# Kernel tuning notes

Measured on AMD Instinct MI355X. Metric: run time of the kernel, lower is better.

## Reference

```python
import jax, jax.numpy as jnp
import numpy as np
from jax import lax

SUB, NSUB, FRAME, COND, FEAT, PEMB = 40, 4, 160, 256, 20, 64
B, NB_FRAMES = 64, 100
T = NB_FRAMES + 4  # two valid k=3 convs drop 4 frames


def setup_inputs() -> dict:
    keys = iter(jax.random.split(jax.random.key(0), 40))
    def W(shape, fan_in):
        return jax.random.normal(next(keys), shape, jnp.float32) / np.float32(np.sqrt(fan_in))
    z = lambda *s: jnp.zeros(s, jnp.float32)
    inp = {
        'features': jax.random.normal(next(keys), (B, T, FEAT), jnp.float32),
        'period': jax.random.randint(next(keys), (B, T), 32, 256, jnp.int32),
        'nb_frames': NB_FRAMES,
        'rand_shift': jax.random.uniform(next(keys), (B, 1), jnp.float32),
        'pembed': 0.1 * jax.random.normal(next(keys), (256, PEMB), jnp.float32),
        'fd1_w': W((FEAT + PEMB, COND), FEAT + PEMB), 'fd1_b': z(COND),
        'conv1_w': W((COND, COND, 3), 3 * COND), 'conv1_b': z(COND),
        'conv2_w': W((COND, COND, 3), 3 * COND), 'conv2_b': z(COND),
        'fd2_w': W((COND, COND), COND), 'fd2_b': z(COND),
        'sd1_w': W((3 * SUB + COND, COND), 3 * SUB + COND), 'sd1_b': z(COND),
        'sd2_w': W((COND, COND), COND), 'sd2_b': z(COND),
        'g1_wi': W((COND, 3 * COND), COND), 'g1_bi': z(3 * COND),
        'g1_wh': W((COND, 3 * COND), COND), 'g1_bh': z(3 * COND),
        'g2_wi': W((COND, 3 * COND), COND), 'g2_bi': z(3 * COND),
        'g2_wh': W((COND, 3 * COND), COND), 'g2_bh': z(3 * COND),
        'g3_wi': W((COND, 3 * COND), COND), 'g3_bi': z(3 * COND),
        'g3_wh': W((COND, 3 * COND), COND), 'g3_bh': z(3 * COND),
        'out_w': W((COND, SUB), COND), 'out_b': z(SUB),
    }
    return inp


def _gru(x, h, wi, bi, wh, bh):
    # torch GRUCell gate order: r, z, n
    gi = x @ wi + bi
    gh = h @ wh + bh
    i_r, i_z, i_n = jnp.split(gi, 3, axis=1)
    h_r, h_z, h_n = jnp.split(gh, 3, axis=1)
    r = jax.nn.sigmoid(i_r + h_r)
    zt = jax.nn.sigmoid(i_z + h_z)
    n = jnp.tanh(i_n + r * h_n)
    return (1.0 - zt) * n + zt * h


def _conv1d_valid(x, w, b):
    # x: (B, C, T), w: (O, I, 3)
    y = lax.conv_general_dilated(x, w, (1,), 'VALID', dimension_numbers=('NCH', 'OIH', 'NCH'))
    return y + b[None, :, None]


def _forward(features, rand_shift, pembed, fd1_w, fd1_b, conv1_w, conv1_b, conv2_w, conv2_b,
             fd2_w, fd2_b, sd1_w, sd1_b, sd2_w, sd2_b,
             g1_wi, g1_bi, g1_wh, g1_bh, g2_wi, g2_bi, g2_wh, g2_bh, g3_wi, g3_bi, g3_wh, g3_bh,
             out_w, out_b, period, nb_frames):
    b = features.shape[0]
    two_pi = np.float32(2.0 * np.pi)
    # --- phase embedding (gen_phase_embedding on period[:, 3:-1]) ---
    p = period[:, 3:-1].astype(jnp.float32)              # (B, nb_frames)
    w0 = two_pi / p
    w0_shift = jnp.concatenate([two_pi * rand_shift / FRAME, w0[:, :-1]], axis=1)
    cum_phase = FRAME * jnp.cumsum(w0_shift, axis=1)     # (B, nb_frames)
    fine = w0[:, :, None] * jnp.arange(FRAME, dtype=jnp.float32)
    embed = (cum_phase[:, :, None] + fine).reshape(b, nb_frames * NSUB, SUB)
    phase_real = jnp.cos(embed)
    phase_imag = jnp.sin(embed)
    # --- conditioning network ---
    pe = pembed[period]                                  # (B, T, PEMB)
    t = jnp.tanh(jnp.concatenate([features, pe], axis=-1) @ fd1_w + fd1_b)
    x = t.transpose(0, 2, 1)                             # (B, COND, T)
    x = jnp.tanh(_conv1d_valid(x, conv1_w, conv1_b))
    x = jnp.tanh(_conv1d_valid(x, conv2_w, conv2_b))
    cond = jnp.tanh(x.transpose(0, 2, 1) @ fd2_w + fd2_b)  # (B, T-4, COND)
    cond_steps = jnp.repeat(cond[:, :nb_frames], NSUB, axis=1)  # (B, steps, COND)
    xs = (cond_steps.transpose(1, 0, 2), phase_real.transpose(1, 0, 2), phase_imag.transpose(1, 0, 2))
    h0 = jnp.zeros((b, COND), features.dtype)
    prev0 = jnp.zeros((b, SUB), features.dtype)

    def step(carry, inp):
        prev, h1, h2, h3 = carry
        c, pr, pi = inp
        tt = jnp.tanh(jnp.concatenate([c, prev, pr, pi], axis=1) @ sd1_w + sd1_b)
        tt = jnp.tanh(tt @ sd2_w + sd2_b)
        h1 = _gru(tt, h1, g1_wi, g1_bi, g1_wh, g1_bh)
        h2 = _gru(h1, h2, g2_wi, g2_bi, g2_wh, g2_bh)
        h3 = _gru(h2, h3, g3_wi, g3_bi, g3_wh, g3_bh)
        out = jnp.tanh(h3 @ out_w + out_b)
        return (out, h1, h2, h3), out

    (_, h1, h2, h3), outs = lax.scan(step, (prev0, h0, h0, h0), xs)
    sig = outs.transpose(1, 0, 2).reshape(b, -1)         # (B, nb_frames*FRAME)
    return sig, (h1, h2, h3)


def reference(features, period, nb_frames, rand_shift, pembed, fd1_w, fd1_b, conv1_w, conv1_b,
              conv2_w, conv2_b, fd2_w, fd2_b, sd1_w, sd1_b, sd2_w, sd2_b,
              g1_wi, g1_bi, g1_wh, g1_bh, g2_wi, g2_bi, g2_wh, g2_bh, g3_wi, g3_bi, g3_wh, g3_bh,
              out_w, out_b):
    return _forward(features, rand_shift, pembed, fd1_w, fd1_b, conv1_w, conv1_b, conv2_w, conv2_b,
                    fd2_w, fd2_b, sd1_w, sd1_b, sd2_w, sd2_b,
                    g1_wi, g1_bi, g1_wh, g1_bh, g2_wi, g2_bi, g2_wh, g2_bh,
                    g3_wi, g3_bi, g3_wh, g3_bh, out_w, out_b, period, nb_frames)
```

## Files before the change

kernel.cpp:

```cpp
#include <hip/hip_runtime.h>
#include <hip/hip_bf16.h>
#include <math.h>

#define B_ 64
#define T_ 104
#define FEAT_ 20
#define PEMB_ 64
#define COND_ 256
#define SUB_ 40
#define NBF_ 100
#define STEPS_ 400

typedef short short8 __attribute__((ext_vector_type(8)));
typedef float floatx4 __attribute__((ext_vector_type(4)));

__device__ inline unsigned short f2bf(float x){
  unsigned int u = __float_as_uint(x);
  unsigned int r = (u + 0x7fffu + ((u >> 16) & 1u)) >> 16;
  return (unsigned short)r;
}
__device__ inline float fast_tanh(float x){
  float e = __expf(2.f*x);
  return 1.f - 2.f*__builtin_amdgcn_rcpf(e + 1.f);
}
__device__ inline float fast_sigm(float x){
  return __builtin_amdgcn_rcpf(1.f + __expf(-x));
}
__device__ inline floatx4 mfma16(short8 a, short8 b, floatx4 c){
  return __builtin_amdgcn_mfma_f32_16x16x32_bf16(a, b, c, 0, 0, 0);
}
__device__ inline unsigned long long ld_coh_u64(const unsigned long long* p){
  return __hip_atomic_load(p, __ATOMIC_RELAXED, __HIP_MEMORY_SCOPE_AGENT);
}
__device__ inline unsigned int ld_coh_u32(const unsigned int* p){
  return __hip_atomic_load(p, __ATOMIC_RELAXED, __HIP_MEMORY_SCOPE_AGENT);
}
__device__ inline void st_coh_u32(unsigned int* p, unsigned int v){
  __hip_atomic_store(p, v, __ATOMIC_RELAXED, __HIP_MEMORY_SCOPE_AGENT);
}
__device__ inline void st_coh_u16(unsigned short* p, unsigned short v){
  unsigned int vv = v;
  asm volatile("global_store_short %0, %1, off sc0 sc1" :: "v"(p), "v"(vv) : "memory");
}

#define FLAG_IDX(st, g, sl) ((((st)*4 + (g))*16 + (sl))*16)

__device__ inline void wave0_wait(const unsigned int* fb, unsigned int tgt,
                                  int wave, int lane){
  if (wave == 0){
    for (;;){
      unsigned int v = 0xFFFFFFFFu;
      if (lane < 16) v = ld_coh_u32(fb + lane*16);
      #pragma unroll
      for (int off = 1; off < 64; off <<= 1)
        v = min(v, (unsigned int)__shfl_xor((int)v, off, 64));
      if (v >= tgt) break;
      __builtin_amdgcn_s_sleep(1);
    }
  }
}

__global__ void k_phase(const int* __restrict__ period, const float* __restrict__ rshift,
                        float* __restrict__ pr, float* __restrict__ pi){
  int b = blockIdx.x;
  __shared__ float cumf[NBF_], w0f[NBF_];
  if (threadIdx.x == 0){
    double acc = 2.0*M_PI*(double)rshift[b];
    for (int f = 0; f < NBF_; ++f){
      double w0 = 2.0*M_PI/(double)period[b*T_ + 3 + f];
      cumf[f] = (float)fmod(acc, 2.0*M_PI);
      w0f[f] = (float)w0;
      acc += 160.0*w0;
    }
  }
  __syncthreads();
  for (int e = threadIdx.x; e < NBF_*160; e += blockDim.x){
    int f = e/160, j = e - f*160;
    float ph = cumf[f] + w0f[f]*(float)j;
    int s = f*4 + j/40, u = j%40;
    pr[((size_t)b*STEPS_ + s)*SUB_ + u] = cosf(ph);
    pi[((size_t)b*STEPS_ + s)*SUB_ + u] = sinf(ph);
  }
}

__global__ void k_prep(const float* __restrict__ c1w, const float* __restrict__ c2w,
                       float* __restrict__ w1t, float* __restrict__ w2t,
                       unsigned int* __restrict__ flags, unsigned int* __restrict__ bufs){
  size_t tid = (size_t)blockIdx.x*blockDim.x + threadIdx.x;
  size_t nt = (size_t)gridDim.x*blockDim.x;
  for (size_t e = tid; e < 4096; e += nt) st_coh_u32(flags + e, 0u);
  for (size_t e = tid; e < 65536; e += nt) st_coh_u32(bufs + e, 0u);
  for (size_t e = tid; e < 768u*256u; e += nt){
    int kk = (int)(e >> 8), o = (int)(e & 255);
    int i = kk & 255, kc = kk >> 8;
    w1t[e] = c1w[(size_t)o*768 + i*3 + kc];
    w2t[e] = c2w[(size_t)o*768 + i*3 + kc];
  }
}

template<int MODE>
__global__ __launch_bounds__(256) void k_gemm(
    const float* __restrict__ a0, const float* __restrict__ a1, const float* __restrict__ a2,
    const int* __restrict__ ip,
    const float* __restrict__ Bm, const float* __restrict__ bias, float* __restrict__ C)
{
  constexpr int KT = (MODE==0) ? 6 : (MODE==1||MODE==2) ? 48 : (MODE==3) ? 16 : 21;
  __shared__ float As[16][68];
  __shared__ float Bs[16][68];
  int tid = threadIdx.x;
  int m0 = blockIdx.x*64, n0 = blockIdx.y*64;
  int tx = tid & 15, ty = tid >> 4;
  float acc[4][4] = {};
  int am = m0 + (tid >> 2);
  int akq = (tid & 3)*4;
  int bk = tid >> 4;
  int bn4 = (tid & 15)*4;

  for (int kt = 0; kt < KT; ++kt){
    int kbase = kt*16;
    float av[4];
    {
      int k0 = kbase + akq;
      if constexpr (MODE==0){
        if (k0 < 20){
          const float* p = a0 + (size_t)am*FEAT_ + k0;
          #pragma unroll
          for (int u=0;u<4;++u) av[u] = p[u];
        } else if (k0 < 84){
          const float* p = a1 + (size_t)ip[am]*PEMB_ + (k0-20);
          #pragma unroll
          for (int u=0;u<4;++u) av[u] = p[u];
        } else { av[0]=av[1]=av[2]=av[3]=0.f; }
      } else if constexpr (MODE==1){
        int b = am/102, t2 = am - b*102;
        int i = k0 & 255, kc = k0 >> 8;
        const float* p = a0 + ((size_t)(b*T_ + t2 + kc))*COND_ + i;
        #pragma unroll
        for (int u=0;u<4;++u) av[u] = p[u];
      } else if constexpr (MODE==2){
        int b = am/100, t2 = am - b*100;
        int i = k0 & 255, kc = k0 >> 8;
        const float* p = a0 + ((size_t)(b*102 + t2 + kc))*COND_ + i;
        #pragma unroll
        for (int u=0;u<4;++u) av[u] = p[u];
      } else if constexpr (MODE==3){
        const float* p = a0 + (size_t)am*COND_ + k0;
        #pragma unroll
        for (int u=0;u<4;++u) av[u] = p[u];
      } else {
        int b = am/400, s = am - b*400;
        const float* p;
        if (k0 < 256)      p = a0 + ((size_t)(b*100 + (s>>2)))*COND_ + k0;
        else if (k0 < 296) p = a1 + ((size_t)(b*400 + s))*SUB_ + (k0-256);
        else               p = a2 + ((size_t)(b*400 + s))*SUB_ + (k0-296);
        #pragma unroll
        for (int u=0;u<4;++u) av[u] = p[u];
      }
    }
    float bv[4];
    {
      int kB = kbase + bk;
      if constexpr (MODE==0){
        if (kB < 84){
          const float* p = Bm + (size_t)kB*256 + n0 + bn4;
          #pragma unroll
          for (int u=0;u<4;++u) bv[u] = p[u];
        } else { bv[0]=bv[1]=bv[2]=bv[3]=0.f; }
      } else if constexpr (MODE==4){
        int krow = (kB < 256) ? kB : kB + 40;
        const float* p = Bm + (size_t)krow*256 + n0 + bn4;
        #pragma unroll
        for (int u=0;u<4;++u) bv[u] = p[u];
      } else {
        const float* p = Bm + (size_t)kB*256 + n0 + bn4;
        #pragma unroll
        for (int u=0;u<4;++u) bv[u] = p[u];
      }
    }
    #pragma unroll
    for (int u=0;u<4;++u) As[akq+u][tid>>2] = av[u];
    #pragma unroll
    for (int u=0;u<4;++u) Bs[bk][bn4+u] = bv[u];
    __syncthreads();
    #pragma unroll
    for (int k = 0; k < 16; ++k){
      float a4[4], b4[4];
      #pragma unroll
      for (int i=0;i<4;++i) a4[i] = As[k][ty*4+i];
      #pragma unroll
      for (int j=0;j<4;++j) b4[j] = Bs[k][tx*4+j];
      #pragma unroll
      for (int i=0;i<4;++i)
        #pragma unroll
        for (int j=0;j<4;++j)
          acc[i][j] += a4[i]*b4[j];
    }
    __syncthreads();
  }
  #pragma unroll
  for (int i=0;i<4;++i){
    int m = m0 + ty*4 + i;
    #pragma unroll
    for (int j=0;j<4;++j){
      int n = n0 + tx*4 + j;
      float v = acc[i][j] + bias[n];
      if constexpr (MODE == 4){
        int b = m/400, s = m - b*400;
        C[((size_t)s*64 + b)*256 + n] = v;
      } else {
        C[(size_t)m*256 + n] = fast_tanh(v);
      }
    }
  }
}

__global__ __launch_bounds__(256, 1) void k_scan(
  const float* __restrict__ sd1_w, const float* __restrict__ sd2_w, const float* __restrict__ sd2_b,
  const float* __restrict__ g1_wi, const float* __restrict__ g1_bi, const float* __restrict__ g1_wh, const float* __restrict__ g1_bh,
  const float* __restrict__ g2_wi, const float* __restrict__ g2_bi, const float* __restrict__ g2_wh, const float* __restrict__ g2_bh,
  const float* __restrict__ g3_wi, const float* __restrict__ g3_bi, const float* __restrict__ g3_wh, const float* __restrict__ g3_bh,
  const float* __restrict__ out_w, const float* __restrict__ out_b,
  const float* __restrict__ tt1p,
  unsigned short* __restrict__ tt2buf, unsigned short* __restrict__ h1buf,
  unsigned short* __restrict__ h2buf, unsigned short* __restrict__ h3buf,
  unsigned int* __restrict__ flags, float* __restrict__ out)
{
  __shared__ __align__(16) char smem[65536];
  int tid = threadIdx.x;
  int lane = tid & 63, wave = tid >> 6;
  int q = lane >> 4, nI = lane & 15;
  int bI = blockIdx.x;
  int g = bI >> 6, rr = bI & 63;
  int set = rr >> 4, sl = rr & 15;
  int b0 = g*16;

  if (set == 0){
    char* outwF = smem;
    char* sd1p0 = smem + 24576;
    char* sd1p1 = smem + 40960;
    char* sd2F  = smem + 45056;
    char* stage = smem + 53248;
    char* prevl = smem + 61440;
    int col1 = sl*16 + nI;
    const unsigned int* fb3 = flags + FLAG_IDX(3, g, 0);
    unsigned int* myflag = flags + FLAG_IDX(0, g, sl);

    for (int t = wave; t < 24; t += 4){
      int nt = t >> 3, kk = t & 7;
      int c = nt*16 + nI;
      unsigned short v[8];
      #pragma unroll
      for (int j = 0; j < 8; ++j){
        int k = kk*32 + q*8 + j;
        v[j] = (c < 40) ? f2bf(out_w[(size_t)k*40 + c]) : (unsigned short)0;
      }
      *(short8*)(outwF + (t*64 + lane)*16) = *(short8*)v;
    }
    for (int t = wave; t < 16; t += 4){
      unsigned short v[8];
      #pragma unroll
      for (int j = 0; j < 8; ++j){
        int k = q*8 + j;
        v[j] = f2bf(sd1_w[(size_t)(256+k)*256 + t*16 + nI]);
      }
      *(short8*)(sd1p0 + (t*64 + lane)*16) = *(short8*)v;
    }
    {
      int nt = tid >> 4, ln = tid & 15;
      unsigned short v[8];
      #pragma unroll
      for (int j = 0; j < 8; ++j)
        v[j] = f2bf(sd1_w[(size_t)(256+32+j)*256 + nt*16 + ln]);
      *(short8*)(sd1p1 + tid*16) = *(short8*)v;
    }
    for (int t = wave; t < 8; t += 4){
      unsigned short v[8];
      #pragma unroll
      for (int j = 0; j < 8; ++j){
        int k = t*32 + q*8 + j;
        v[j] = f2bf(sd2_w[(size_t)k*256 + col1]);
      }
      *(short8*)(sd2F + (t*64 + lane)*16) = *(short8*)v;
    }
    for (int e = tid; e < 16*72; e += 256) *(unsigned short*)(prevl + e*2) = 0;
    float bout = 0.f;
    if (wave < 3){ int c = wave*16 + nI; if (c < 40) bout = out_b[c]; }
    float bsd2 = sd2_b[col1];
    __syncthreads();

    for (int s = 0; s <= STEPS_; ++s){
      float t1r[16];
      if (s < STEPS_){
        const float* tb = tt1p + ((size_t)s*64 + b0)*256;
        #pragma unroll
        for (int ii = 0; ii < 4; ++ii){
          int c = (wave*4 + ii)*16 + nI;
          #pragma unroll
          for (int i = 0; i < 4; ++i)
            t1r[ii*4+i] = tb[(q*4+i)*256 + c];
        }
      }
      if (s > 0){
        wave0_wait(fb3, (unsigned)s, wave, lane);
        __syncthreads();
        const unsigned short* h3s = h3buf + ((size_t)((s+1)&1)*4 + g)*4096;
        for (int c = tid; c < 512; c += 256){
          int row = c >> 5, gc = c & 31;
          const unsigned long long* sp = (const unsigned long long*)(h3s + row*256 + gc*8);
          unsigned long long w0 = ld_coh_u64(sp), w1 = ld_coh_u64(sp+1);
          unsigned long long* dst = (unsigned long long*)(stage + (row*32 + (gc ^ (row & 7)))*16);
          dst[0]=w0; dst[1]=w1;
        }
        __syncthreads();
        if (wave < 3){
          floatx4 acc = {0.f,0.f,0.f,0.f};
          #pragma unroll
          for (int kk = 0; kk < 8; ++kk){
            short8 a = *(const short8*)(stage + (nI*32 + ((kk*4+q) ^ (nI & 7)))*16);
            short8 b = *(const short8*)(outwF + ((wave*8+kk)*64 + lane)*16);
            acc = mfma16(a, b, acc);
          }
          int c = wave*16 + nI;
          #pragma unroll
          for (int i = 0; i < 4; ++i){
            int row = q*4 + i;
            float pv = (c < 40) ? fast_tanh(acc[i] + bout) : 0.f;
            *(unsigned short*)(prevl + (row*72 + c)*2) = f2bf(pv);
            if (sl == 0 && c < 40)
              out[(size_t)(b0+row)*16000 + (size_t)(s-1)*40 + c] = pv;
          }
        }
      }
      if (s == STEPS_) break;
      __syncthreads();
      #pragma unroll
      for (int ii = 0; ii < 4; ++ii){
        int nt = wave*4 + ii;
        floatx4 acc = {0.f,0.f,0.f,0.f};
        short8 a0v = *(const short8*)(prevl + nI*144 + q*16);
        short8 b0v = *(const short8*)(sd1p0 + (nt*64 + lane)*16);
        acc = mfma16(a0v, b0v, acc);
        short8 a1v = *(const short8*)(prevl + nI*144 + 64 + q*16);
        short8 b1v = {0,0,0,0,0,0,0,0};
        if (q == 0) b1v = *(const short8*)(sd1p1 + (nt*16 + nI)*16);
        acc = mfma16(a1v, b1v, acc);
        int c = nt*16 + nI;
        #pragma unroll
        for (int i = 0; i < 4; ++i){
          int row = q*4 + i;
          float tv = fast_tanh(acc[i] + t1r[ii*4+i]);
          int gc = c >> 3;
          *(unsigned short*)(stage + (row*32 + (gc ^ (row & 7)))*16 + (c & 7)*2) = f2bf(tv);
        }
      }
      __syncthreads();
      if (wave == 0){
        floatx4 acc = {0.f,0.f,0.f,0.f};
        #pragma unroll
        for (int kk = 0; kk < 8; ++kk){
          short8 a = *(const short8*)(stage + (nI*32 + ((kk*4+q) ^ (nI & 7)))*16);
          short8 b = *(const short8*)(sd2F + (kk*64 + lane)*16);
          acc = mfma16(a, b, acc);
        }
        unsigned short* t2 = tt2buf + ((size_t)(s&1)*4 + g)*4096;
        #pragma unroll
        for (int i = 0; i < 4; ++i){
          int row = q*4 + i;
          st_coh_u16(&t2[row*256 + col1], f2bf(fast_tanh(acc[i] + bsd2)));
        }
      }
      __syncthreads();
      if (tid == 0) st_coh_u32(myflag, (unsigned)(s+1));
    }
  } else {
    int gi_ = set - 1;
    const float* wi = (gi_==0) ? g1_wi : (gi_==1) ? g2_wi : g3_wi;
    const float* wh = (gi_==0) ? g1_wh : (gi_==1) ? g2_wh : g3_wh;
    const float* bi = (gi_==0) ? g1_bi : (gi_==1) ? g2_bi : g3_bi;
    const float* bh = (gi_==0) ? g1_bh : (gi_==1) ? g2_bh : g3_bh;
    unsigned short* hOut = (gi_==0) ? h1buf : (gi_==1) ? h2buf : h3buf;
    const unsigned short* xBase = (gi_==0) ? tt2buf : (gi_==1) ? h1buf : h2buf;
    char* wlds  = smem;
    char* stage = smem + 49152;
    int hc0 = sl*16;
    const unsigned int* fbOwn  = flags + FLAG_IDX(set, g, 0);
    const unsigned int* fbPrev = flags + FLAG_IDX(set-1, g, 0);
    unsigned int* myflag = flags + FLAG_IDX(set, g, sl);

    for (int t = wave; t < 48; t += 4){
      unsigned short v[8];
      #pragma unroll
      for (int j = 0; j < 8; ++j){
        float w;
        if (t < 32){
          int k512 = (t & 15)*32 + q*8 + j;
          int col = ((t < 16) ? 0 : 256) + hc0 + nI;
          w = (k512 < 256) ? wi[(size_t)k512*768 + col] : wh[(size_t)(k512-256)*768 + col];
        } else if (t < 40){
          int k = (t-32)*32 + q*8 + j;
          w = wi[(size_t)k*768 + 512 + hc0 + nI];
        } else {
          int k = (t-40)*32 + q*8 + j;
          w = wh[(size_t)k*768 + 512 + hc0 + nI];
        }
        v[j] = f2bf(w);
      }
      *(short8*)(wlds + (t*64 + lane)*16) = *(short8*)v;
    }
    float br = 0.f, bz = 0.f, bin = 0.f, bhn = 0.f;
    if (wave == 0){
      int cg = hc0 + nI;
      br  = bi[cg] + bh[cg];
      bz  = bi[256+cg] + bh[256+cg];
      bin = bi[512+cg];
      bhn = bh[512+cg];
    }
    floatx4 hst = {0.f,0.f,0.f,0.f};
    __syncthreads();

    for (int s = 0; s < STEPS_; ++s){
      if (s > 0) wave0_wait(fbOwn, (unsigned)s, wave, lane);
      __syncthreads();
      const unsigned short* hs = hOut + ((size_t)((s+1)&1)*4 + g)*4096;
      for (int c = tid; c < 512; c += 256){
        int row = c >> 5, gc = c & 31;
        const unsigned long long* sp = (const unsigned long long*)(hs + row*256 + gc*8);
        unsigned long long w0 = ld_coh_u64(sp), w1 = ld_coh_u64(sp+1);
        unsigned long long* dst = (unsigned long long*)(stage + (row*64 + ((32+gc) ^ (row & 7)))*16);
        dst[0]=w0; dst[1]=w1;
      }
      __syncthreads();
      floatx4 acc = {0.f,0.f,0.f,0.f};
      if (wave < 2){
        int tb = wave*16;
        #pragma unroll
        for (int kt = 8; kt < 16; ++kt){
          short8 a = *(const short8*)(stage + (nI*64 + ((kt*4+q) ^ (nI & 7)))*16);
          short8 b = *(const short8*)(wlds + ((tb+kt)*64 + lane)*16);
          acc = mfma16(a, b, acc);
        }
      } else if (wave == 3){
        #pragma unroll
        for (int kt = 0; kt < 8; ++kt){
          short8 a = *(const short8*)(stage + (nI*64 + ((32 + kt*4+q) ^ (nI & 7)))*16);
          short8 b = *(const short8*)(wlds + ((40+kt)*64 + lane)*16);
          acc = mfma16(a, b, acc);
        }
      }
      wave0_wait(fbPrev, (unsigned)(s+1), wave, lane);
      __syncthreads();
      const unsigned short* xs = xBase + ((size_t)(s&1)*4 + g)*4096;
      for (int c = tid; c < 512; c += 256){
        int row = c >> 5, gc = c & 31;
        const unsigned long long* sp = (const unsigned long long*)(xs + row*256 + gc*8);
        unsigned long long w0 = ld_coh_u64(sp), w1 = ld_coh_u64(sp+1);
        unsigned long long* dst = (unsigned long long*)(stage + (row*64 + (gc ^ (row & 7)))*16);
        dst[0]=w0; dst[1]=w1;
      }
      __syncthreads();
      if (wave < 2){
        int tb = wave*16;
        #pragma unroll
        for (int kt = 0; kt < 8; ++kt){
          short8 a = *(const short8*)(stage + (nI*64 + ((kt*4+q) ^ (nI & 7)))*16);
          short8 b = *(const short8*)(wlds + ((tb+kt)*64 + lane)*16);
          acc = mfma16(a, b, acc);
        }
      } else if (wave == 2){
        #pragma unroll
        for (int kt = 0; kt < 8; ++kt){
          short8 a = *(const short8*)(stage + (nI*64 + ((kt*4+q) ^ (nI & 7)))*16);
          short8 b = *(const short8*)(wlds + ((32+kt)*64 + lane)*16);
          acc = mfma16(a, b, acc);
        }
      }
      __syncthreads();
      float* ex = (float*)stage;
      if (wave >= 1){
        float* dst = ex + (wave-1)*256;
        #pragma unroll
        for (int i = 0; i < 4; ++i) dst[(q*4+i)*16 + nI] = acc[i];
      }
      __syncthreads();
      if (wave == 0){
        unsigned short* ho = hOut + ((size_t)(s&1)*4 + g)*4096;
        #pragma unroll
        for (int i = 0; i < 4; ++i){
          int row = q*4 + i;
          float zr  = ex[0*256 + row*16 + nI];
          float inr = ex[1*256 + row*16 + nI];
          float hnr = ex[2*256 + row*16 + nI];
          float rv = fast_sigm(acc[i] + br);
          float zv = fast_sigm(zr + bz);
          float nv = fast_tanh(inr + bin + rv*(hnr + bhn));
          float hv = (1.f - zv)*nv + zv*hst[i];
          hst[i] = hv;
          st_coh_u16(&ho[row*256 + hc0 + nI], f2bf(hv));
          if (s == STEPS_-1)
            out[1024000 + gi_*16384 + (size_t)(b0+row)*256 + hc0 + nI] = hv;
        }
      }
      __syncthreads();
      if (tid == 0) st_coh_u32(myflag, (unsigned)(s+1));
    }
  }
}

extern "C" void kernel_launch(void* const* d_in, const int* in_sizes, int n_in,
                              void* d_out, int out_size, void* d_ws, size_t ws_size,
                              hipStream_t stream){
  (void)in_sizes; (void)n_in; (void)out_size; (void)ws_size;
  const float* features = (const float*)d_in[0];
  const int*   period   = (const int*)d_in[1];
  const float* rshift   = (const float*)d_in[3];
  const float* pembed   = (const float*)d_in[4];
  const float* fd1_w = (const float*)d_in[5];  const float* fd1_b = (const float*)d_in[6];
  const float* c1w   = (const float*)d_in[7];  const float* c1b   = (const float*)d_in[8];
  const float* c2w   = (const float*)d_in[9];  const float* c2b   = (const float*)d_in[10];
  const float* fd2_w = (const float*)d_in[11]; const float* fd2_b = (const float*)d_in[12];
  const float* sd1_w = (const float*)d_in[13]; const float* sd1_b = (const float*)d_in[14];
  const float* sd2_w = (const float*)d_in[15]; const float* sd2_b = (const float*)d_in[16];
  const float* g1_wi = (const float*)d_in[17]; const float* g1_bi = (const float*)d_in[18];
  const float* g1_wh = (const float*)d_in[19]; const float* g1_bh = (const float*)d_in[20];
  const float* g2_wi = (const float*)d_in[21]; const float* g2_bi = (const float*)d_in[22];
  const float* g2_wh = (const float*)d_in[23]; const float* g2_bh = (const float*)d_in[24];
  const float* g3_wi = (const float*)d_in[25]; const float* g3_bi = (const float*)d_in[26];
  const float* g3_wh = (const float*)d_in[27]; const float* g3_bh = (const float*)d_in[28];
  const float* out_w = (const float*)d_in[29]; const float* out_b = (const float*)d_in[30];

  char* ws = (char*)d_ws;
  size_t off = 0;
  auto alloc = [&](size_t bytes)->char*{
    char* p = ws + off; off += (bytes + 255) & ~(size_t)255; return p;
  };
  unsigned int*  flags  = (unsigned int*)alloc(16384);
  unsigned short* tt2b  = (unsigned short*)alloc(65536);
  unsigned short* h1b   = (unsigned short*)alloc(65536);
  unsigned short* h2b   = (unsigned short*)alloc(65536);
  unsigned short* h3b   = (unsigned short*)alloc(65536);
  float* tt1p = (float*)alloc((size_t)B_*STEPS_*COND_*4);
  float* pr   = (float*)alloc((size_t)B_*STEPS_*SUB_*4);
  float* pi   = (float*)alloc((size_t)B_*STEPS_*SUB_*4);
  float* tbuf = (float*)alloc((size_t)B_*T_*COND_*4);
  float* x1   = (float*)alloc((size_t)B_*102*COND_*4);
  float* x2   = (float*)alloc((size_t)B_*100*COND_*4);
  float* cb   = (float*)alloc((size_t)B_*100*COND_*4);
  float* w1t  = (float*)alloc((size_t)768*256*4);
  float* w2t  = (float*)alloc((size_t)768*256*4);

  k_phase<<<64, 256, 0, stream>>>(period, rshift, pr, pi);
  k_prep<<<256, 256, 0, stream>>>(c1w, c2w, w1t, w2t, flags, (unsigned int*)tt2b);
  k_gemm<0><<<dim3(104,4), 256, 0, stream>>>(features, pembed, nullptr, period, fd1_w, fd1_b, tbuf);
  k_gemm<1><<<dim3(102,4), 256, 0, stream>>>(tbuf, nullptr, nullptr, nullptr, w1t, c1b, x1);
  k_gemm<2><<<dim3(100,4), 256, 0, stream>>>(x1, nullptr, nullptr, nullptr, w2t, c2b, x2);
  k_gemm<3><<<dim3(100,4), 256, 0, stream>>>(x2, nullptr, nullptr, nullptr, fd2_w, fd2_b, cb);
  k_gemm<4><<<dim3(400,4), 256, 0, stream>>>(cb, pr, pi, nullptr, sd1_w, sd1_b, tt1p);
  k_scan<<<256, 256, 0, stream>>>(sd1_w, sd2_w, sd2_b,
                                  g1_wi, g1_bi, g1_wh, g1_bh,
                                  g2_wi, g2_bi, g2_wh, g2_bh,
                                  g3_wi, g3_bi, g3_wh, g3_bh,
                                  out_w, out_b, tt1p,
                                  tt2b, h1b, h2b, h3b, flags, (float*)d_out);
}
```

Measured before the change: 4.606 ms.

## Replace flag-based inter-block sync with step-tagged data words polled directly

Each bf16 value exchanged between scan blocks is now stored as a 32-bit word with the step number in the upper half. Consumers spin directly on the data until every tag reaches the target step, instead of waiting on a separate flag array and then reloading the data. This removes a flag store, a barrier and a dependent load round-trip from each stage handoff. The GRU gate epilogue is also spread across all 256 threads rather than one wave. The cost is twice the message bytes, and every thread now polls the buffers instead of only wave 0.

```diff
diff --git a/kernel.cpp b/kernel.cpp
--- a/kernel.cpp
+++ b/kernel.cpp
@@ -13,6 +13,7 @@
 
 typedef short short8 __attribute__((ext_vector_type(8)));
 typedef float floatx4 __attribute__((ext_vector_type(4)));
+typedef unsigned int uintx4 __attribute__((ext_vector_type(4)));
 
 __device__ inline unsigned short f2bf(float x){
   unsigned int u = __float_as_uint(x);
@@ -32,32 +33,44 @@
 __device__ inline unsigned long long ld_coh_u64(const unsigned long long* p){
   return __hip_atomic_load(p, __ATOMIC_RELAXED, __HIP_MEMORY_SCOPE_AGENT);
 }
-__device__ inline unsigned int ld_coh_u32(const unsigned int* p){
-  return __hip_atomic_load(p, __ATOMIC_RELAXED, __HIP_MEMORY_SCOPE_AGENT);
-}
 __device__ inline void st_coh_u32(unsigned int* p, unsigned int v){
   __hip_atomic_store(p, v, __ATOMIC_RELAXED, __HIP_MEMORY_SCOPE_AGENT);
 }
-__device__ inline void st_coh_u16(unsigned short* p, unsigned short v){
-  unsigned int vv = v;
-  asm volatile("global_store_short %0, %1, off sc0 sc1" :: "v"(p), "v"(vv) : "memory");
-}
-
-#define FLAG_IDX(st, g, sl) ((((st)*4 + (g))*16 + (sl))*16)
-
-__device__ inline void wave0_wait(const unsigned int* fb, unsigned int tgt,
-                                  int wave, int lane){
-  if (wave == 0){
-    for (;;){
-      unsigned int v = 0xFFFFFFFFu;
-      if (lane < 16) v = ld_coh_u32(fb + lane*16);
-      #pragma unroll
-      for (int off = 1; off < 64; off <<= 1)
-        v = min(v, (unsigned int)__shfl_xor((int)v, off, 64));
-      if (v >= tgt) break;
-      __builtin_amdgcn_s_sleep(1);
-    }
-  }
+
+template<int STRIDE, int GCOFF>
+__device__ inline void poll_stage(const unsigned int* __restrict__ src, char* dst,
+                                  unsigned tgt, int tid){
+  int c0 = tid, c1 = tid + 256;
+  int r0 = c0 >> 5, g0 = c0 & 31;
+  int r1 = c1 >> 5, g1 = c1 & 31;
+  const unsigned long long* p0 = (const unsigned long long*)src + (r0*128 + g0*4);
+  const unsigned long long* p1 = (const unsigned long long*)src + (r1*128 + g1*4);
+  unsigned long long w[8];
+  for (;;){
+    #pragma unroll
+    for (int u = 0; u < 4; ++u) w[u]   = ld_coh_u64(p0 + u);
+    #pragma unroll
+    for (int u = 0; u < 4; ++u) w[4+u] = ld_coh_u64(p1 + u);
+    unsigned mt = 0xFFFFu;
+    #pragma unroll
+    for (int u = 0; u < 8; ++u){
+      unsigned t0 = (unsigned)(w[u] >> 16) & 0xFFFFu;
+      unsigned t1 = (unsigned)(w[u] >> 48);
+      mt = min(mt, min(t0, t1));
+    }
+    if (__all((int)(mt >= tgt))) break;
+    __builtin_amdgcn_s_sleep(1);
+  }
+  unsigned int pk0[4], pk1[4];
+  #pragma unroll
+  for (int u = 0; u < 4; ++u){
+    pk0[u] = ((unsigned int)w[u]   & 0xFFFFu) | ((unsigned int)(w[u]   >> 32) << 16);
+    pk1[u] = ((unsigned int)w[4+u] & 0xFFFFu) | ((unsigned int)(w[4+u] >> 32) << 16);
+  }
+  uintx4 v0 = {pk0[0], pk0[1], pk0[2], pk0[3]};
+  uintx4 v1 = {pk1[0], pk1[1], pk1[2], pk1[3]};
+  *(uintx4*)(dst + (size_t)(r0*STRIDE + ((GCOFF + g0) ^ (r0 & 7)))*16) = v0;
+  *(uintx4*)(dst + (size_t)(r1*STRIDE + ((GCOFF + g1) ^ (r1 & 7)))*16) = v1;
 }
 
 __global__ void k_phase(const int* __restrict__ period, const float* __restrict__ rshift,
@@ -85,11 +98,10 @@
 
 __global__ void k_prep(const float* __restrict__ c1w, const float* __restrict__ c2w,
                        float* __restrict__ w1t, float* __restrict__ w2t,
-                       unsigned int* __restrict__ flags, unsigned int* __restrict__ bufs){
+                       unsigned int* __restrict__ msg){
   size_t tid = (size_t)blockIdx.x*blockDim.x + threadIdx.x;
   size_t nt = (size_t)gridDim.x*blockDim.x;
-  for (size_t e = tid; e < 4096; e += nt) st_coh_u32(flags + e, 0u);
-  for (size_t e = tid; e < 65536; e += nt) st_coh_u32(bufs + e, 0u);
+  for (size_t e = tid; e < 131072; e += nt) st_coh_u32(msg + e, 0u);
   for (size_t e = tid; e < 768u*256u; e += nt){
     int kk = (int)(e >> 8), o = (int)(e & 255);
     int i = kk & 255, kc = kk >> 8;
@@ -221,9 +233,9 @@
   const float* __restrict__ g3_wi, const float* __restrict__ g3_bi, const float* __restrict__ g3_wh, const float* __restrict__ g3_bh,
   const float* __restrict__ out_w, const float* __restrict__ out_b,
   const float* __restrict__ tt1p,
-  unsigned short* __restrict__ tt2buf, unsigned short* __restrict__ h1buf,
-  unsigned short* __restrict__ h2buf, unsigned short* __restrict__ h3buf,
-  unsigned int* __restrict__ flags, float* __restrict__ out)
+  unsigned int* __restrict__ tt2buf, unsigned int* __restrict__ h1buf,
+  unsigned int* __restrict__ h2buf, unsigned int* __restrict__ h3buf,
+  float* __restrict__ out)
 {
   __shared__ __align__(16) char smem[65536];
   int tid = threadIdx.x;
@@ -242,8 +254,6 @@
     char* stage = smem + 53248;
     char* prevl = smem + 61440;
     int col1 = sl*16 + nI;
-    const unsigned int* fb3 = flags + FLAG_IDX(3, g, 0);
-    unsigned int* myflag = flags + FLAG_IDX(0, g, sl);
 
     for (int t = wave; t < 24; t += 4){
       int nt = t >> 3, kk = t & 7;
@@ -301,16 +311,8 @@
         }
       }
       if (s > 0){
-        wave0_wait(fb3, (unsigned)s, wave, lane);
-        __syncthreads();
-        const unsigned short* h3s = h3buf + ((size_t)((s+1)&1)*4 + g)*4096;
-        for (int c = tid; c < 512; c += 256){
-          int row = c >> 5, gc = c & 31;
-          const unsigned long long* sp = (const unsigned long long*)(h3s + row*256 + gc*8);
-          unsigned long long w0 = ld_coh_u64(sp), w1 = ld_coh_u64(sp+1);
-          unsigned long long* dst = (unsigned long long*)(stage + (row*32 + (gc ^ (row & 7)))*16);
-          dst[0]=w0; dst[1]=w1;
-        }
+        const unsigned int* h3s = h3buf + ((size_t)((s+1)&1)*4 + g)*4096;
+        poll_stage<32,0>(h3s, stage, (unsigned)s, tid);
         __syncthreads();
         if (wave < 3){
           floatx4 acc = {0.f,0.f,0.f,0.f};
@@ -362,15 +364,15 @@
           short8 b = *(const short8*)(sd2F + (kk*64 + lane)*16);
           acc = mfma16(a, b, acc);
         }
-        unsigned short* t2 = tt2buf + ((size_t)(s&1)*4 + g)*4096;
+        unsigned int* t2 = tt2buf + ((size_t)(s&1)*4 + g)*4096;
+        unsigned int tg = (unsigned)(s+1) << 16;
         #pragma unroll
         for (int i = 0; i < 4; ++i){
           int row = q*4 + i;
-          st_coh_u16(&t2[row*256 + col1], f2bf(fast_tanh(acc[i] + bsd2)));
-        }
-      }
-      __syncthreads();
-      if (tid == 0) st_coh_u32(myflag, (unsigned)(s+1));
+          st_coh_u32(&t2[row*256 + col1], tg | (unsigned)f2bf(fast_tanh(acc[i] + bsd2)));
+        }
+      }
+      __syncthreads();
     }
   } else {
     int gi_ = set - 1;
@@ -378,14 +380,11 @@
     const float* wh = (gi_==0) ? g1_wh : (gi_==1) ? g2_wh : g3_wh;
     const float* bi = (gi_==0) ? g1_bi : (gi_==1) ? g2_bi : g3_bi;
     const float* bh = (gi_==0) ? g1_bh : (gi_==1) ? g2_bh : g3_bh;
-    unsigned short* hOut = (gi_==0) ? h1buf : (gi_==1) ? h2buf : h3buf;
-    const unsigned short* xBase = (gi_==0) ? tt2buf : (gi_==1) ? h1buf : h2buf;
+    unsigned int* hOut = (gi_==0) ? h1buf : (gi_==1) ? h2buf : h3buf;
+    const unsigned int* xBase = (gi_==0) ? tt2buf : (gi_==1) ? h1buf : h2buf;
     char* wlds  = smem;
     char* stage = smem + 49152;
     int hc0 = sl*16;
-    const unsigned int* fbOwn  = flags + FLAG_IDX(set, g, 0);
-    const unsigned int* fbPrev = flags + FLAG_IDX(set-1, g, 0);
-    unsigned int* myflag = flags + FLAG_IDX(set, g, sl);
 
     for (int t = wave; t < 48; t += 4){
       unsigned short v[8];
@@ -407,28 +406,18 @@
       }
       *(short8*)(wlds + (t*64 + lane)*16) = *(short8*)v;
     }
-    float br = 0.f, bz = 0.f, bin = 0.f, bhn = 0.f;
-    if (wave == 0){
-      int cg = hc0 + nI;
-      br  = bi[cg] + bh[cg];
-      bz  = bi[256+cg] + bh[256+cg];
-      bin = bi[512+cg];
-      bhn = bh[512+cg];
-    }
-    floatx4 hst = {0.f,0.f,0.f,0.f};
+    int erow = tid >> 4, ecol = tid & 15;
+    int cg = hc0 + ecol;
+    float br  = bi[cg] + bh[cg];
+    float bz  = bi[256+cg] + bh[256+cg];
+    float bin = bi[512+cg];
+    float bhn = bh[512+cg];
+    float hstate = 0.f;
     __syncthreads();
 
     for (int s = 0; s < STEPS_; ++s){
-      if (s > 0) wave0_wait(fbOwn, (unsigned)s, wave, lane);
-      __syncthreads();
-      const unsigned short* hs = hOut + ((size_t)((s+1)&1)*4 + g)*4096;
-      for (int c = tid; c < 512; c += 256){
-        int row = c >> 5, gc = c & 31;
-        const unsigned long long* sp = (const unsigned long long*)(hs + row*256 + gc*8);
-        unsigned long long w0 = ld_coh_u64(sp), w1 = ld_coh_u64(sp+1);
-        unsigned long long* dst = (unsigned long long*)(stage + (row*64 + ((32+gc) ^ (row & 7)))*16);
-        dst[0]=w0; dst[1]=w1;
-      }
+      const unsigned int* hs = hOut + ((size_t)((s+1)&1)*4 + g)*4096;
+      poll_stage<64,32>(hs, stage, (unsigned)s, tid);
       __syncthreads();
       floatx4 acc = {0.f,0.f,0.f,0.f};
       if (wave < 2){
@@ -447,16 +436,8 @@
           acc = mfma16(a, b, acc);
         }
       }
-      wave0_wait(fbPrev, (unsigned)(s+1), wave, lane);
-      __syncthreads();
-      const unsigned short* xs = xBase + ((size_t)(s&1)*4 + g)*4096;
-      for (int c = tid; c < 512; c += 256){
-        int row = c >> 5, gc = c & 31;
-        const unsigned long long* sp = (const unsigned long long*)(xs + row*256 + gc*8);
-        unsigned long long w0 = ld_coh_u64(sp), w1 = ld_coh_u64(sp+1);
-        unsigned long long* dst = (unsigned long long*)(stage + (row*64 + (gc ^ (row & 7)))*16);
-        dst[0]=w0; dst[1]=w1;
-      }
+      const unsigned int* xs = xBase + ((size_t)(s&1)*4 + g)*4096;
+      poll_stage<64,0>(xs, stage, (unsigned)(s+1), tid);
       __syncthreads();
       if (wave < 2){
         int tb = wave*16;
@@ -476,32 +457,24 @@
       }
       __syncthreads();
       float* ex = (float*)stage;
-      if (wave >= 1){
-        float* dst = ex + (wave-1)*256;
+      {
+        float* dst = ex + wave*256;
         #pragma unroll
         for (int i = 0; i < 4; ++i) dst[(q*4+i)*16 + nI] = acc[i];
       }
       __syncthreads();
-      if (wave == 0){
-        unsigned short* ho = hOut + ((size_t)(s&1)*4 + g)*4096;
-        #pragma unroll
-        for (int i = 0; i < 4; ++i){
-          int row = q*4 + i;
-          float zr  = ex[0*256 + row*16 + nI];
-          float inr = ex[1*256 + row*16 + nI];
-          float hnr = ex[2*256 + row*16 + nI];
-          float rv = fast_sigm(acc[i] + br);
-          float zv = fast_sigm(zr + bz);
-          float nv = fast_tanh(inr + bin + rv*(hnr + bhn));
-          float hv = (1.f - zv)*nv + zv*hst[i];
-          hst[i] = hv;
-          st_coh_u16(&ho[row*256 + hc0 + nI], f2bf(hv));
-          if (s == STEPS_-1)
-            out[1024000 + gi_*16384 + (size_t)(b0+row)*256 + hc0 + nI] = hv;
-        }
-      }
-      __syncthreads();
-      if (tid == 0) st_coh_u32(myflag, (unsigned)(s+1));
+      {
+        float rv  = fast_sigm(ex[tid] + br);
+        float zv  = fast_sigm(ex[256 + tid] + bz);
+        float nv  = fast_tanh(ex[512 + tid] + bin + rv*(ex[768 + tid] + bhn));
+        float hv  = (1.f - zv)*nv + zv*hstate;
+        hstate = hv;
+        unsigned int* ho = hOut + ((size_t)(s&1)*4 + g)*4096;
+        st_coh_u32(&ho[erow*256 + cg], ((unsigned)(s+1) << 16) | (unsigned)f2bf(hv));
+        if (s == STEPS_-1)
+          out[1024000 + gi_*16384 + (size_t)(b0+erow)*256 + cg] = hv;
+      }
+      __syncthreads();
     }
   }
 }
@@ -533,11 +506,11 @@
   auto alloc = [&](size_t bytes)->char*{
     char* p = ws + off; off += (bytes + 255) & ~(size_t)255; return p;
   };
-  unsigned int*  flags  = (unsigned int*)alloc(16384);
-  unsigned short* tt2b  = (unsigned short*)alloc(65536);
-  unsigned short* h1b   = (unsigned short*)alloc(65536);
-  unsigned short* h2b   = (unsigned short*)alloc(65536);
-  unsigned short* h3b   = (unsigned short*)alloc(65536);
+  unsigned int* msg = (unsigned int*)alloc(524288);
+  unsigned int* tt2b = msg;
+  unsigned int* h1b  = msg + 32768;
+  unsigned int* h2b  = msg + 65536;
+  unsigned int* h3b  = msg + 98304;
   float* tt1p = (float*)alloc((size_t)B_*STEPS_*COND_*4);
   float* pr   = (float*)alloc((size_t)B_*STEPS_*SUB_*4);
   float* pi   = (float*)alloc((size_t)B_*STEPS_*SUB_*4);
@@ -549,7 +522,7 @@
   float* w2t  = (float*)alloc((size_t)768*256*4);
 
   k_phase<<<64, 256, 0, stream>>>(period, rshift, pr, pi);
-  k_prep<<<256, 256, 0, stream>>>(c1w, c2w, w1t, w2t, flags, (unsigned int*)tt2b);
+  k_prep<<<256, 256, 0, stream>>>(c1w, c2w, w1t, w2t, msg);
   k_gemm<0><<<dim3(104,4), 256, 0, stream>>>(features, pembed, nullptr, period, fd1_w, fd1_b, tbuf);
   k_gemm<1><<<dim3(102,4), 256, 0, stream>>>(tbuf, nullptr, nullptr, nullptr, w1t, c1b, x1);
   k_gemm<2><<<dim3(100,4), 256, 0, stream>>>(x1, nullptr, nullptr, nullptr, w2t, c2b, x2);
@@ -560,5 +533,5 @@
                                   g2_wi, g2_bi, g2_wh, g2_bh,
                                   g3_wi, g3_bi, g3_wh, g3_bh,
                                   out_w, out_b, tt1p,
-                                  tt2b, h1b, h2b, h3b, flags, (float*)d_out);
-}
+                                  tt2b, h1b, h2b, h3b, (float*)d_out);
+}
```

Result: faster. 4.506 ms (-2.2%).
